# Optimization experiments

Measured on AMD Instinct MI355X. Metric: run time of the kernel, lower is better.

## Reference

```python
import jax, jax.numpy as jnp
import numpy as np


def setup_inputs() -> dict:
    key = jax.random.key(0)
    ks = jax.random.split(key, 7)
    n, d_in, d_h = 1024, 1024, 512
    scale = 1.0 / np.sqrt(d_in)
    return {
        "vectors": jax.random.normal(ks[0], (n, d_in), dtype=jnp.float32),
        "W_h": jax.random.normal(ks[1], (d_h, d_in), dtype=jnp.float32) * scale,
        "b_h": jax.random.normal(ks[2], (d_h,), dtype=jnp.float32) * 0.01,
        "W_m": jax.random.normal(ks[3], (d_h, d_in), dtype=jnp.float32) * scale,
        "b_m": jax.random.normal(ks[4], (d_h,), dtype=jnp.float32) * 0.01,
        "w2": jax.random.normal(ks[5], (d_h,), dtype=jnp.float32) * (1.0 / np.sqrt(d_h)),
        "b2": jax.random.normal(ks[6], (1,), dtype=jnp.float32) * 0.01,
    }


def reference(vectors, W_h, b_h, W_m, b_m, w2, b2):
    # Two linear projections: [n, d_h]
    h = vectors @ W_h.T + b_h  # head representations
    m = vectors @ W_m.T + b_m  # modifier representations
    # Pairwise broadcast add: pair[i, j, :] = h[i] + m[j]  -> [n, n, d_h]
    pair = jnp.tanh(h[:, None, :] + m[None, :, :])
    # Linear to scalar + squeeze -> [n, n]
    scores = jnp.einsum("ijh,h->ij", pair, w2) + b2[0]
    return scores
```

## Files before the change

### kernel.cpp

```cpp
#include <hip/hip_runtime.h>
#include <hip/hip_bf16.h>

#define D_IN  1024
#define D_H   512
#define L2E2  2.885390081777927f
#define ECLAMP 15.0f

typedef _Float16 half8 __attribute__((ext_vector_type(8)));
typedef _Float16 half4v __attribute__((ext_vector_type(4)));
typedef float f32x4 __attribute__((ext_vector_type(4)));

__global__ __launch_bounds__(256) void cvt_kernel(
    const float* __restrict__ V,
    const float* __restrict__ Wh, const float* __restrict__ Wm,
    _Float16* __restrict__ Vh, _Float16* __restrict__ Wf)
{
  const int idx = blockIdx.x * 256 + threadIdx.x;
  {
    float4 x = ((const float4*)V)[idx];
    half4v o = { (_Float16)x.x, (_Float16)x.y, (_Float16)x.z, (_Float16)x.w };
    ((half4v*)Vh)[idx] = o;
  }
  {
    const float4* p = (idx < 131072) ? ((const float4*)Wh + idx)
                                     : ((const float4*)Wm + (idx - 131072));
    float4 x = *p;
    half4v o = { (_Float16)x.x, (_Float16)x.y, (_Float16)x.z, (_Float16)x.w };
    ((half4v*)Wf)[idx] = o;
  }
}

__global__ __launch_bounds__(256, 4) void proj_mfma_kernel(
    const _Float16* __restrict__ Vh, const _Float16* __restrict__ Wf,
    const float* __restrict__ bh, const float* __restrict__ bm,
    float* __restrict__ C)
{
  __shared__ float red[4][32][34];

  const int tid  = threadIdx.x;
  const int lane = tid & 63;
  const int wid  = tid >> 6;
  const int bid  = blockIdx.x;
  const int swz  = (bid & 7) * 128 + (bid >> 3);
  const int i0   = (swz & 31) * 32;
  const int j0   = (swz >> 5) * 32;
  const int r16  = lane & 15;
  const int kg   = lane >> 4;
  const int kb   = wid * 256;

  const _Float16* A0 = Vh + (size_t)(i0 + r16) * 1024 + kb + kg*8;
  const _Float16* A1 = A0 + 16 * 1024;
  const _Float16* B0 = Wf + (size_t)(j0 + r16) * 1024 + kb + kg*8;
  const _Float16* B1 = B0 + 16 * 1024;

  f32x4 acc00 = {0.f,0.f,0.f,0.f}, acc01 = acc00, acc10 = acc00, acc11 = acc00;
  #pragma unroll 4
  for (int k0 = 0; k0 < 256; k0 += 32) {
    half8 a0 = *(const half8*)(A0 + k0);
    half8 a1 = *(const half8*)(A1 + k0);
    half8 b0 = *(const half8*)(B0 + k0);
    half8 b1 = *(const half8*)(B1 + k0);
    acc00 = __builtin_amdgcn_mfma_f32_16x16x32_f16(a0, b0, acc00, 0, 0, 0);
    acc01 = __builtin_amdgcn_mfma_f32_16x16x32_f16(a0, b1, acc01, 0, 0, 0);
    acc10 = __builtin_amdgcn_mfma_f32_16x16x32_f16(a1, b0, acc10, 0, 0, 0);
    acc11 = __builtin_amdgcn_mfma_f32_16x16x32_f16(a1, b1, acc11, 0, 0, 0);
  }

  #pragma unroll
  for (int fi = 0; fi < 2; ++fi) {
    #pragma unroll
    for (int fj = 0; fj < 2; ++fj) {
      const f32x4 acc = (fi == 0) ? (fj == 0 ? acc00 : acc01)
                                  : (fj == 0 ? acc10 : acc11);
      #pragma unroll
      for (int rr = 0; rr < 4; ++rr)
        red[wid][16*fi + 4*kg + rr][16*fj + r16] = acc[rr];
    }
  }
  __syncthreads();

  const int row = tid >> 3;
  const int c4  = (tid & 7) * 4;
  const float* biasp = (j0 < D_H) ? (bh + j0) : (bm + (j0 - D_H));
  float4 bias = *(const float4*)(biasp + c4);
  float4 o;
  #pragma unroll
  for (int q = 0; q < 4; ++q) {
    float s = red[0][row][c4+q] + red[1][row][c4+q]
            + red[2][row][c4+q] + red[3][row][c4+q];
    float x = (s + (&bias.x)[q]) * L2E2;
    x = fminf(fmaxf(x, -ECLAMP), ECLAMP);
    (&o.x)[q] = __builtin_amdgcn_exp2f(x);
  }
  *(float4*)(C + (size_t)(i0 + row) * 1024 + j0 + c4) = o;
}

__global__ __launch_bounds__(256) void proj_kernel(
    const float* __restrict__ V,
    const float* __restrict__ Wh, const float* __restrict__ bh,
    const float* __restrict__ Wm, const float* __restrict__ bm,
    float* __restrict__ C)
{
  __shared__ float As[16][68];
  __shared__ float Bs[16][68];

  const int tid = threadIdx.x;
  const int i0  = (blockIdx.x & 15) * 64, j0 = (blockIdx.x >> 4) * 64;
  const int ti  = tid >> 4, tj = tid & 15;
  const int sr  = tid >> 2;
  const int sk  = (tid & 3) << 2;

  const float* Wbase = (j0 < D_H) ? (Wh + (size_t)j0 * D_IN)
                                  : (Wm + (size_t)(j0 - D_H) * D_IN);
  const float* biasp = (j0 < D_H) ? (bh + j0) : (bm + (j0 - D_H));

  const float* arow = V     + (size_t)(i0 + sr) * D_IN + sk;
  const float* brow = Wbase + (size_t)sr        * D_IN + sk;

  float acc[4][4] = {};
  for (int k0 = 0; k0 < D_IN; k0 += 16) {
    float4 av = *(const float4*)(arow + k0);
    float4 bv = *(const float4*)(brow + k0);
    As[sk+0][sr] = av.x; As[sk+1][sr] = av.y; As[sk+2][sr] = av.z; As[sk+3][sr] = av.w;
    Bs[sk+0][sr] = bv.x; Bs[sk+1][sr] = bv.y; Bs[sk+2][sr] = bv.z; Bs[sk+3][sr] = bv.w;
    __syncthreads();
    #pragma unroll
    for (int kk = 0; kk < 16; ++kk) {
      float4 a = *(const float4*)&As[kk][4*ti];
      float4 b = *(const float4*)&Bs[kk][4*tj];
      #pragma unroll
      for (int x = 0; x < 4; ++x)
        #pragma unroll
        for (int y = 0; y < 4; ++y)
          acc[x][y] = fmaf((&a.x)[x], (&b.x)[y], acc[x][y]);
    }
    __syncthreads();
  }

  const int jl = 4 * tj;
  #pragma unroll
  for (int aa = 0; aa < 4; ++aa) {
    const int i = i0 + 4*ti + aa;
    float4 o;
    #pragma unroll
    for (int bb = 0; bb < 4; ++bb) {
      float x = (acc[aa][bb] + biasp[jl+bb]) * L2E2;
      x = fminf(fmaxf(x, -ECLAMP), ECLAMP);
      (&o.x)[bb] = __builtin_amdgcn_exp2f(x);
    }
    *(float4*)(C + (size_t)i * 1024 + j0 + jl) = o;
  }
}

__global__ __launch_bounds__(256, 2) void score_kernel(
    const float* __restrict__ C,
    const float* __restrict__ w2,
    const float* __restrict__ b2,
    float* __restrict__ out)
{
  __shared__ float hs[2][64][34];
  __shared__ float ms[2][32][34];
  __shared__ float wred[4];

  const int tid = threadIdx.x;
  const int bi  = blockIdx.x & 15;
  const int bj  = blockIdx.x >> 4;
  const int i0  = bi * 64, j0 = bj * 32;
  const int ti  = tid >> 4, tj = tid & 15;

  const int sr  = tid >> 3;
  const int sk  = (tid & 7) << 2;

  float sw = 0.f;
  for (int t = tid; t < D_H; t += 256) sw += w2[t];
  #pragma unroll
  for (int off = 32; off > 0; off >>= 1) sw += __shfl_down(sw, off, 64);
  if ((tid & 63) == 0) wred[tid >> 6] = sw;

  const float* hrow0 = C + (size_t)(i0 + sr)      * 1024 + sk;
  const float* hrow1 = C + (size_t)(i0 + sr + 32) * 1024 + sk;
  const float* mrow  = C + (size_t)(j0 + sr) * 1024 + D_H + sk;

  float4 hv0 = *(const float4*)(hrow0);
  float4 hv1 = *(const float4*)(hrow1);
  float4 mv  = *(const float4*)(mrow);

  float acc[4][2] = {};
  int p = 0;

  for (int k0 = 0; k0 < D_H; k0 += 32) {
    *(float2*)&hs[p][sr][sk]          = make_float2(hv0.x, hv0.y);
    *(float2*)&hs[p][sr][sk + 2]      = make_float2(hv0.z, hv0.w);
    *(float2*)&hs[p][sr + 32][sk]     = make_float2(hv1.x, hv1.y);
    *(float2*)&hs[p][sr + 32][sk + 2] = make_float2(hv1.z, hv1.w);
    *(float2*)&ms[p][sr][sk]          = make_float2(mv.x, mv.y);
    *(float2*)&ms[p][sr][sk + 2]      = make_float2(mv.z, mv.w);
    __syncthreads();

    if (k0 + 32 < D_H) {
      hv0 = *(const float4*)(hrow0 + k0 + 32);
      hv1 = *(const float4*)(hrow1 + k0 + 32);
      mv  = *(const float4*)(mrow  + k0 + 32);
    }

    #pragma unroll
    for (int g = 0; g < 8; ++g) {
      const int kk = 4 * g;
      const float wA = w2[k0 + kk + 0];
      const float wB = w2[k0 + kk + 1];
      const float wC = w2[k0 + kk + 2];
      const float wD = w2[k0 + kk + 3];
      float2 em_[2][2], eh_[4][2];
      #pragma unroll
      for (int c = 0; c < 2; ++c) {
        em_[c][0] = *(const float2*)&ms[p][tj + 16*c][kk];
        em_[c][1] = *(const float2*)&ms[p][tj + 16*c][kk + 2];
      }
      #pragma unroll
      for (int a = 0; a < 4; ++a) {
        eh_[a][0] = *(const float2*)&hs[p][ti + 16*a][kk];
        eh_[a][1] = *(const float2*)&hs[p][ti + 16*a][kk + 2];
      }
      #pragma unroll
      for (int a = 0; a < 4; ++a)
        #pragma unroll
        for (int c = 0; c < 2; ++c) {
          float uA = fmaf(eh_[a][0].x, em_[c][0].x, 1.f);
          float uB = fmaf(eh_[a][0].y, em_[c][0].y, 1.f);
          float uC = fmaf(eh_[a][1].x, em_[c][1].x, 1.f);
          float uD = fmaf(eh_[a][1].y, em_[c][1].y, 1.f);
          float dAB = uA * uB, dCD = uC * uD;
          float nAB = fmaf(wB, uA, wA * uB);
          float nCD = fmaf(wD, uC, wC * uD);
          float den = dAB * dCD;
          float num = fmaf(nCD, dAB, nAB * dCD);
          acc[a][c] = fmaf(num, __builtin_amdgcn_rcpf(den), acc[a][c]);
        }
    }
    p ^= 1;
  }

  const float base = b2[0] + wred[0] + wred[1] + wred[2] + wred[3];
  #pragma unroll
  for (int a = 0; a < 4; ++a) {
    const int i = i0 + ti + 16*a;
    #pragma unroll
    for (int c = 0; c < 2; ++c) {
      const int j = j0 + tj + 16*c;
      out[(size_t)i * 1024 + j] = fmaf(-2.f, acc[a][c], base);
    }
  }
}

extern "C" void kernel_launch(void* const* d_in, const int* in_sizes, int n_in,
                              void* d_out, int out_size, void* d_ws, size_t ws_size,
                              hipStream_t stream) {
  const float* V  = (const float*)d_in[0];
  const float* Wh = (const float*)d_in[1];
  const float* bh = (const float*)d_in[2];
  const float* Wm = (const float*)d_in[3];
  const float* bm = (const float*)d_in[4];
  const float* w2 = (const float*)d_in[5];
  const float* b2 = (const float*)d_in[6];
  float* outp = (float*)d_out;

  char* ws = (char*)d_ws;
  float* C = (float*)ws;

  if (ws_size >= (size_t)(8u << 20)) {
    _Float16* Vh = (_Float16*)(ws + (4u << 20));
    _Float16* Wf = (_Float16*)(ws + (6u << 20));
    cvt_kernel<<<dim3(1024), dim3(256), 0, stream>>>(V, Wh, Wm, Vh, Wf);
    proj_mfma_kernel<<<dim3(1024), dim3(256), 0, stream>>>(Vh, Wf, bh, bm, C);
  } else {
    proj_kernel<<<dim3(256), dim3(256), 0, stream>>>(V, Wh, bh, Wm, bm, C);
  }
  score_kernel<<<dim3(512), dim3(256), 0, stream>>>(C, w2, b2, outp);
}
```

Before: 80.94 us.

## Fuse fp16 conversion into projection and split score reduction over hidden dim

Removes the separate conversion kernel: the MFMA projection now loads fp32 inputs and converts to fp16 in registers. The score kernel is split four ways along the hidden dimension with 64x64 tiles and 1024 blocks, each writing fp16 partial sums that a new combine kernel adds into the output. This aims to raise parallelism and per-thread reuse in the dominant score stage. The cost is an extra launch, partial-sum memory traffic, and precision loss from storing partials in fp16.

Measured after the change: 85.35 us. +5.5%, slower.

```diff
diff --git a/kernel.cpp b/kernel.cpp
--- a/kernel.cpp
+++ b/kernel.cpp
@@ -10,28 +10,18 @@
 typedef _Float16 half4v __attribute__((ext_vector_type(4)));
 typedef float f32x4 __attribute__((ext_vector_type(4)));
 
-__global__ __launch_bounds__(256) void cvt_kernel(
+static __device__ __forceinline__ half8 cvt8(float4 lo, float4 hi) {
+  half8 r;
+  r[0] = (_Float16)lo.x; r[1] = (_Float16)lo.y;
+  r[2] = (_Float16)lo.z; r[3] = (_Float16)lo.w;
+  r[4] = (_Float16)hi.x; r[5] = (_Float16)hi.y;
+  r[6] = (_Float16)hi.z; r[7] = (_Float16)hi.w;
+  return r;
+}
+
+__global__ __launch_bounds__(256, 2) void proj_fused_kernel(
     const float* __restrict__ V,
     const float* __restrict__ Wh, const float* __restrict__ Wm,
-    _Float16* __restrict__ Vh, _Float16* __restrict__ Wf)
-{
-  const int idx = blockIdx.x * 256 + threadIdx.x;
-  {
-    float4 x = ((const float4*)V)[idx];
-    half4v o = { (_Float16)x.x, (_Float16)x.y, (_Float16)x.z, (_Float16)x.w };
-    ((half4v*)Vh)[idx] = o;
-  }
-  {
-    const float4* p = (idx < 131072) ? ((const float4*)Wh + idx)
-                                     : ((const float4*)Wm + (idx - 131072));
-    float4 x = *p;
-    half4v o = { (_Float16)x.x, (_Float16)x.y, (_Float16)x.z, (_Float16)x.w };
-    ((half4v*)Wf)[idx] = o;
-  }
-}
-
-__global__ __launch_bounds__(256, 4) void proj_mfma_kernel(
-    const _Float16* __restrict__ Vh, const _Float16* __restrict__ Wf,
     const float* __restrict__ bh, const float* __restrict__ bm,
     float* __restrict__ C)
 {
@@ -48,18 +38,21 @@
   const int kg   = lane >> 4;
   const int kb   = wid * 256;
 
-  const _Float16* A0 = Vh + (size_t)(i0 + r16) * 1024 + kb + kg*8;
-  const _Float16* A1 = A0 + 16 * 1024;
-  const _Float16* B0 = Wf + (size_t)(j0 + r16) * 1024 + kb + kg*8;
-  const _Float16* B1 = B0 + 16 * 1024;
+  const float* Wbase = (j0 < D_H) ? (Wh + (size_t)j0 * D_IN)
+                                  : (Wm + (size_t)(j0 - D_H) * D_IN);
+
+  const float* A0 = V     + (size_t)(i0 + r16) * 1024 + kb + kg*8;
+  const float* A1 = A0 + 16 * 1024;
+  const float* B0 = Wbase + (size_t)r16        * 1024 + kb + kg*8;
+  const float* B1 = B0 + 16 * 1024;
 
   f32x4 acc00 = {0.f,0.f,0.f,0.f}, acc01 = acc00, acc10 = acc00, acc11 = acc00;
   #pragma unroll 4
   for (int k0 = 0; k0 < 256; k0 += 32) {
-    half8 a0 = *(const half8*)(A0 + k0);
-    half8 a1 = *(const half8*)(A1 + k0);
-    half8 b0 = *(const half8*)(B0 + k0);
-    half8 b1 = *(const half8*)(B1 + k0);
+    half8 a0 = cvt8(*(const float4*)(A0 + k0), *(const float4*)(A0 + k0 + 4));
+    half8 a1 = cvt8(*(const float4*)(A1 + k0), *(const float4*)(A1 + k0 + 4));
+    half8 b0 = cvt8(*(const float4*)(B0 + k0), *(const float4*)(B0 + k0 + 4));
+    half8 b1 = cvt8(*(const float4*)(B1 + k0), *(const float4*)(B1 + k0 + 4));
     acc00 = __builtin_amdgcn_mfma_f32_16x16x32_f16(a0, b0, acc00, 0, 0, 0);
     acc01 = __builtin_amdgcn_mfma_f32_16x16x32_f16(a0, b1, acc01, 0, 0, 0);
     acc10 = __builtin_amdgcn_mfma_f32_16x16x32_f16(a1, b0, acc10, 0, 0, 0);
@@ -95,140 +88,88 @@
   *(float4*)(C + (size_t)(i0 + row) * 1024 + j0 + c4) = o;
 }
 
-__global__ __launch_bounds__(256) void proj_kernel(
-    const float* __restrict__ V,
-    const float* __restrict__ Wh, const float* __restrict__ bh,
-    const float* __restrict__ Wm, const float* __restrict__ bm,
-    float* __restrict__ C)
-{
-  __shared__ float As[16][68];
-  __shared__ float Bs[16][68];
-
-  const int tid = threadIdx.x;
-  const int i0  = (blockIdx.x & 15) * 64, j0 = (blockIdx.x >> 4) * 64;
-  const int ti  = tid >> 4, tj = tid & 15;
-  const int sr  = tid >> 2;
-  const int sk  = (tid & 3) << 2;
-
-  const float* Wbase = (j0 < D_H) ? (Wh + (size_t)j0 * D_IN)
-                                  : (Wm + (size_t)(j0 - D_H) * D_IN);
-  const float* biasp = (j0 < D_H) ? (bh + j0) : (bm + (j0 - D_H));
-
-  const float* arow = V     + (size_t)(i0 + sr) * D_IN + sk;
-  const float* brow = Wbase + (size_t)sr        * D_IN + sk;
-
-  float acc[4][4] = {};
-  for (int k0 = 0; k0 < D_IN; k0 += 16) {
-    float4 av = *(const float4*)(arow + k0);
-    float4 bv = *(const float4*)(brow + k0);
-    As[sk+0][sr] = av.x; As[sk+1][sr] = av.y; As[sk+2][sr] = av.z; As[sk+3][sr] = av.w;
-    Bs[sk+0][sr] = bv.x; Bs[sk+1][sr] = bv.y; Bs[sk+2][sr] = bv.z; Bs[sk+3][sr] = bv.w;
-    __syncthreads();
-    #pragma unroll
-    for (int kk = 0; kk < 16; ++kk) {
-      float4 a = *(const float4*)&As[kk][4*ti];
-      float4 b = *(const float4*)&Bs[kk][4*tj];
-      #pragma unroll
-      for (int x = 0; x < 4; ++x)
-        #pragma unroll
-        for (int y = 0; y < 4; ++y)
-          acc[x][y] = fmaf((&a.x)[x], (&b.x)[y], acc[x][y]);
-    }
-    __syncthreads();
-  }
-
-  const int jl = 4 * tj;
-  #pragma unroll
-  for (int aa = 0; aa < 4; ++aa) {
-    const int i = i0 + 4*ti + aa;
-    float4 o;
-    #pragma unroll
-    for (int bb = 0; bb < 4; ++bb) {
-      float x = (acc[aa][bb] + biasp[jl+bb]) * L2E2;
-      x = fminf(fmaxf(x, -ECLAMP), ECLAMP);
-      (&o.x)[bb] = __builtin_amdgcn_exp2f(x);
-    }
-    *(float4*)(C + (size_t)i * 1024 + j0 + jl) = o;
-  }
-}
-
-__global__ __launch_bounds__(256, 2) void score_kernel(
+__global__ __launch_bounds__(256, 2) void score_q_kernel(
     const float* __restrict__ C,
     const float* __restrict__ w2,
     const float* __restrict__ b2,
-    float* __restrict__ out)
+    _Float16* __restrict__ P0, _Float16* __restrict__ P1,
+    _Float16* __restrict__ P2, _Float16* __restrict__ P3)
 {
-  __shared__ float hs[2][64][34];
-  __shared__ float ms[2][32][34];
+  __shared__ float hs[2][64][36];
+  __shared__ float ms[2][64][36];
   __shared__ float wred[4];
 
-  const int tid = threadIdx.x;
-  const int bi  = blockIdx.x & 15;
-  const int bj  = blockIdx.x >> 4;
-  const int i0  = bi * 64, j0 = bj * 32;
-  const int ti  = tid >> 4, tj = tid & 15;
-
-  const int sr  = tid >> 3;
-  const int sk  = (tid & 7) << 2;
-
-  float sw = 0.f;
-  for (int t = tid; t < D_H; t += 256) sw += w2[t];
-  #pragma unroll
-  for (int off = 32; off > 0; off >>= 1) sw += __shfl_down(sw, off, 64);
-  if ((tid & 63) == 0) wred[tid >> 6] = sw;
-
-  const float* hrow0 = C + (size_t)(i0 + sr)      * 1024 + sk;
-  const float* hrow1 = C + (size_t)(i0 + sr + 32) * 1024 + sk;
-  const float* mrow  = C + (size_t)(j0 + sr) * 1024 + D_H + sk;
+  const int tid  = threadIdx.x;
+  const int b    = blockIdx.x;
+  const int v    = (b & 7) * 128 + (b >> 3);
+  const int tile = v >> 2;
+  const int kh   = v & 3;
+  const int i0   = (tile & 15) * 64;
+  const int j0   = (tile >> 4) * 64;
+  const int kb   = kh * 128;
+  const int ti   = tid >> 4, tj = tid & 15;
+
+  const int sr   = tid >> 3;
+  const int sk   = (tid & 7) << 2;
+
+  if (kh == 0) {
+    float sw = 0.f;
+    for (int t = tid; t < D_H; t += 256) sw += w2[t];
+    #pragma unroll
+    for (int off = 32; off > 0; off >>= 1) sw += __shfl_down(sw, off, 64);
+    if ((tid & 63) == 0) wred[tid >> 6] = sw;
+  }
+
+  const float* hrow0 = C + (size_t)(i0 + sr)      * 1024 + kb + sk;
+  const float* hrow1 = C + (size_t)(i0 + sr + 32) * 1024 + kb + sk;
+  const float* mrow0 = C + (size_t)(j0 + sr)      * 1024 + D_H + kb + sk;
+  const float* mrow1 = C + (size_t)(j0 + sr + 32) * 1024 + D_H + kb + sk;
 
   float4 hv0 = *(const float4*)(hrow0);
   float4 hv1 = *(const float4*)(hrow1);
-  float4 mv  = *(const float4*)(mrow);
-
-  float acc[4][2] = {};
+  float4 mv0 = *(const float4*)(mrow0);
+  float4 mv1 = *(const float4*)(mrow1);
+
+  float acc[4][4] = {};
   int p = 0;
 
-  for (int k0 = 0; k0 < D_H; k0 += 32) {
-    *(float2*)&hs[p][sr][sk]          = make_float2(hv0.x, hv0.y);
-    *(float2*)&hs[p][sr][sk + 2]      = make_float2(hv0.z, hv0.w);
-    *(float2*)&hs[p][sr + 32][sk]     = make_float2(hv1.x, hv1.y);
-    *(float2*)&hs[p][sr + 32][sk + 2] = make_float2(hv1.z, hv1.w);
-    *(float2*)&ms[p][sr][sk]          = make_float2(mv.x, mv.y);
-    *(float2*)&ms[p][sr][sk + 2]      = make_float2(mv.z, mv.w);
+  for (int k0 = 0; k0 < 128; k0 += 32) {
+    *(float4*)&hs[p][sr][sk]      = hv0;
+    *(float4*)&hs[p][sr + 32][sk] = hv1;
+    *(float4*)&ms[p][sr][sk]      = mv0;
+    *(float4*)&ms[p][sr + 32][sk] = mv1;
     __syncthreads();
 
-    if (k0 + 32 < D_H) {
+    if (k0 + 32 < 128) {
       hv0 = *(const float4*)(hrow0 + k0 + 32);
       hv1 = *(const float4*)(hrow1 + k0 + 32);
-      mv  = *(const float4*)(mrow  + k0 + 32);
+      mv0 = *(const float4*)(mrow0 + k0 + 32);
+      mv1 = *(const float4*)(mrow1 + k0 + 32);
     }
 
     #pragma unroll
     for (int g = 0; g < 8; ++g) {
       const int kk = 4 * g;
-      const float wA = w2[k0 + kk + 0];
-      const float wB = w2[k0 + kk + 1];
-      const float wC = w2[k0 + kk + 2];
-      const float wD = w2[k0 + kk + 3];
-      float2 em_[2][2], eh_[4][2];
-      #pragma unroll
-      for (int c = 0; c < 2; ++c) {
-        em_[c][0] = *(const float2*)&ms[p][tj + 16*c][kk];
-        em_[c][1] = *(const float2*)&ms[p][tj + 16*c][kk + 2];
-      }
+      float4 eh[4], em[4];
+      #pragma unroll
+      for (int a = 0; a < 4; ++a)
+        eh[a] = *(const float4*)&hs[p][ti + 16*a][kk];
+      #pragma unroll
+      for (int c = 0; c < 4; ++c)
+        em[c] = *(const float4*)&ms[p][tj + 16*c][kk];
+
+      const float wA = w2[kb + k0 + kk + 0];
+      const float wB = w2[kb + k0 + kk + 1];
+      const float wC = w2[kb + k0 + kk + 2];
+      const float wD = w2[kb + k0 + kk + 3];
       #pragma unroll
       for (int a = 0; a < 4; ++a) {
-        eh_[a][0] = *(const float2*)&hs[p][ti + 16*a][kk];
-        eh_[a][1] = *(const float2*)&hs[p][ti + 16*a][kk + 2];
-      }
-      #pragma unroll
-      for (int a = 0; a < 4; ++a)
         #pragma unroll
-        for (int c = 0; c < 2; ++c) {
-          float uA = fmaf(eh_[a][0].x, em_[c][0].x, 1.f);
-          float uB = fmaf(eh_[a][0].y, em_[c][0].y, 1.f);
-          float uC = fmaf(eh_[a][1].x, em_[c][1].x, 1.f);
-          float uD = fmaf(eh_[a][1].y, em_[c][1].y, 1.f);
+        for (int c = 0; c < 4; ++c) {
+          float uA = fmaf(eh[a].x, em[c].x, 1.f);
+          float uB = fmaf(eh[a].y, em[c].y, 1.f);
+          float uC = fmaf(eh[a].z, em[c].z, 1.f);
+          float uD = fmaf(eh[a].w, em[c].w, 1.f);
           float dAB = uA * uB, dCD = uC * uD;
           float nAB = fmaf(wB, uA, wA * uB);
           float nCD = fmaf(wD, uC, wC * uD);
@@ -236,6 +177,122 @@
           float num = fmaf(nCD, dAB, nAB * dCD);
           acc[a][c] = fmaf(num, __builtin_amdgcn_rcpf(den), acc[a][c]);
         }
+      }
+    }
+    p ^= 1;
+  }
+
+  float base = 0.f;
+  if (kh == 0) base = b2[0] + wred[0] + wred[1] + wred[2] + wred[3];
+  _Float16* Pz = (kh == 0) ? P0 : (kh == 1) ? P1 : (kh == 2) ? P2 : P3;
+  #pragma unroll
+  for (int a = 0; a < 4; ++a) {
+    const int i = i0 + ti + 16*a;
+    #pragma unroll
+    for (int c = 0; c < 4; ++c) {
+      const int j = j0 + tj + 16*c;
+      Pz[(size_t)i * 1024 + j] = (_Float16)fmaf(-2.f, acc[a][c], base);
+    }
+  }
+}
+
+__global__ __launch_bounds__(256) void combine_kernel(
+    const _Float16* __restrict__ P0, const _Float16* __restrict__ P1,
+    const _Float16* __restrict__ P2, const _Float16* __restrict__ P3,
+    float* __restrict__ out)
+{
+  const int idx = blockIdx.x * 256 + threadIdx.x;
+  half4v a = ((const half4v*)P0)[idx];
+  half4v b = ((const half4v*)P1)[idx];
+  half4v c = ((const half4v*)P2)[idx];
+  half4v d = ((const half4v*)P3)[idx];
+  float4 o;
+  #pragma unroll
+  for (int q = 0; q < 4; ++q)
+    (&o.x)[q] = (float)a[q] + (float)b[q] + ((float)c[q] + (float)d[q]);
+  ((float4*)out)[idx] = o;
+}
+
+__global__ __launch_bounds__(256, 2) void score_kernel_r9(
+    const float* __restrict__ C,
+    const float* __restrict__ w2,
+    const float* __restrict__ b2,
+    float* __restrict__ out)
+{
+  __shared__ float hs[2][64][36];
+  __shared__ float ms[2][32][36];
+  __shared__ float wred[4];
+
+  const int tid = threadIdx.x;
+  const int bi  = blockIdx.x & 15;
+  const int bj  = blockIdx.x >> 4;
+  const int i0  = bi * 64, j0 = bj * 32;
+  const int ti  = tid >> 4, tj = tid & 15;
+
+  const int sr  = tid >> 3;
+  const int sk  = (tid & 7) << 2;
+
+  float sw = 0.f;
+  for (int t = tid; t < D_H; t += 256) sw += w2[t];
+  #pragma unroll
+  for (int off = 32; off > 0; off >>= 1) sw += __shfl_down(sw, off, 64);
+  if ((tid & 63) == 0) wred[tid >> 6] = sw;
+
+  const float* hrow0 = C + (size_t)(i0 + sr)      * 1024 + sk;
+  const float* hrow1 = C + (size_t)(i0 + sr + 32) * 1024 + sk;
+  const float* mrow  = C + (size_t)(j0 + sr) * 1024 + D_H + sk;
+
+  float4 hv0 = *(const float4*)(hrow0);
+  float4 hv1 = *(const float4*)(hrow1);
+  float4 mv  = *(const float4*)(mrow);
+
+  float acc[4][2] = {};
+  int p = 0;
+
+  for (int k0 = 0; k0 < D_H; k0 += 32) {
+    *(float4*)&hs[p][sr][sk]      = hv0;
+    *(float4*)&hs[p][sr + 32][sk] = hv1;
+    *(float4*)&ms[p][sr][sk]      = mv;
+    __syncthreads();
+
+    if (k0 + 32 < D_H) {
+      hv0 = *(const float4*)(hrow0 + k0 + 32);
+      hv1 = *(const float4*)(hrow1 + k0 + 32);
+      mv  = *(const float4*)(mrow  + k0 + 32);
+    }
+
+    #pragma unroll
+    for (int g = 0; g < 8; ++g) {
+      const int kk = 4 * g;
+      float4 eh[4];
+      float4 em[2];
+      #pragma unroll
+      for (int a = 0; a < 4; ++a)
+        eh[a] = *(const float4*)&hs[p][ti + 16*a][kk];
+      #pragma unroll
+      for (int c = 0; c < 2; ++c)
+        em[c] = *(const float4*)&ms[p][tj + 16*c][kk];
+
+      const float wA = w2[k0 + kk + 0];
+      const float wB = w2[k0 + kk + 1];
+      const float wC = w2[k0 + kk + 2];
+      const float wD = w2[k0 + kk + 3];
+      #pragma unroll
+      for (int a = 0; a < 4; ++a) {
+        #pragma unroll
+        for (int c = 0; c < 2; ++c) {
+          float uA = fmaf(eh[a].x, em[c].x, 1.f);
+          float uB = fmaf(eh[a].y, em[c].y, 1.f);
+          float uC = fmaf(eh[a].z, em[c].z, 1.f);
+          float uD = fmaf(eh[a].w, em[c].w, 1.f);
+          float dAB = uA * uB, dCD = uC * uD;
+          float nAB = fmaf(wB, uA, wA * uB);
+          float nCD = fmaf(wD, uC, wC * uD);
+          float den = dAB * dCD;
+          float num = fmaf(nCD, dAB, nAB * dCD);
+          acc[a][c] = fmaf(num, __builtin_amdgcn_rcpf(den), acc[a][c]);
+        }
+      }
     }
     p ^= 1;
   }
@@ -267,13 +324,16 @@
   char* ws = (char*)d_ws;
   float* C = (float*)ws;
 
-  if (ws_size >= (size_t)(8u << 20)) {
-    _Float16* Vh = (_Float16*)(ws + (4u << 20));
-    _Float16* Wf = (_Float16*)(ws + (6u << 20));
-    cvt_kernel<<<dim3(1024), dim3(256), 0, stream>>>(V, Wh, Wm, Vh, Wf);
-    proj_mfma_kernel<<<dim3(1024), dim3(256), 0, stream>>>(Vh, Wf, bh, bm, C);
+  proj_fused_kernel<<<dim3(1024), dim3(256), 0, stream>>>(V, Wh, Wm, bh, bm, C);
+
+  if (ws_size >= (size_t)(12u << 20)) {
+    _Float16* P0 = (_Float16*)(ws + (4u << 20));
+    _Float16* P1 = (_Float16*)(ws + (6u << 20));
+    _Float16* P2 = (_Float16*)(ws + (8u << 20));
+    _Float16* P3 = (_Float16*)(ws + (10u << 20));
+    score_q_kernel<<<dim3(1024), dim3(256), 0, stream>>>(C, w2, b2, P0, P1, P2, P3);
+    combine_kernel<<<dim3(1024), dim3(256), 0, stream>>>(P0, P1, P2, P3, outp);
   } else {
-    proj_kernel<<<dim3(256), dim3(256), 0, stream>>>(V, Wh, bh, Wm, bm, C);
-  }
-  score_kernel<<<dim3(512), dim3(256), 0, stream>>>(C, w2, b2, outp);
-}
+    score_kernel_r9<<<dim3(512), dim3(256), 0, stream>>>(C, w2, b2, outp);
+  }
+}
```

## Split score reduction over hidden dim into four partial kernels plus combine

Applied to the files above, without the earlier changes.

Adds a split-K score kernel. Each of 1024 blocks computes a 64x64 output tile over a quarter of the hidden dimension, reading operands straight from global memory without LDS, and writes fp16 partial sums. A combine kernel then adds the four partials into the fp32 output. This raises parallelism and drops LDS staging and barriers, at the cost of an extra launch, extra partial traffic, and fp16 rounding of partials, which risks accuracy. The fallback score kernel also switches to float4 LDS accesses with padding changed to 36.

After: 105.7 us. 1.31x slower.

```diff
diff --git a/kernel.cpp b/kernel.cpp
--- a/kernel.cpp
+++ b/kernel.cpp
@@ -152,14 +152,111 @@
   }
 }
 
-__global__ __launch_bounds__(256, 2) void score_kernel(
+__global__ __launch_bounds__(256, 2) void score_gd_kernel(
+    const float* __restrict__ C,
+    const float* __restrict__ w2,
+    const float* __restrict__ b2,
+    _Float16* __restrict__ P0, _Float16* __restrict__ P1,
+    _Float16* __restrict__ P2, _Float16* __restrict__ P3)
+{
+  __shared__ float wred[4];
+
+  const int tid  = threadIdx.x;
+  const int b    = blockIdx.x;
+  const int v    = (b & 7) * 128 + (b >> 3);
+  const int tile = v >> 2;
+  const int kh   = v & 3;
+  const int i0   = (tile & 15) * 64;
+  const int j0   = (tile >> 4) * 64;
+  const int kb   = kh * 128;
+  const int ti   = tid >> 4, tj = tid & 15;
+
+  if (kh == 0) {
+    float sw = 0.f;
+    for (int t = tid; t < D_H; t += 256) sw += w2[t];
+    #pragma unroll
+    for (int off = 32; off > 0; off >>= 1) sw += __shfl_down(sw, off, 64);
+    if ((tid & 63) == 0) wred[tid >> 6] = sw;
+  }
+  __syncthreads();
+
+  const float* ehb = C + (size_t)(i0 + ti) * 1024 + kb;
+  const float* emb = C + (size_t)(j0 + tj) * 1024 + D_H + kb;
+
+  float acc[4][4] = {};
+
+  #pragma unroll 4
+  for (int g = 0; g < 32; ++g) {
+    const int kk = 4 * g;
+    float4 eh[4], em[4];
+    #pragma unroll
+    for (int a = 0; a < 4; ++a)
+      eh[a] = *(const float4*)(ehb + (size_t)a * 16384 + kk);
+    #pragma unroll
+    for (int c = 0; c < 4; ++c)
+      em[c] = *(const float4*)(emb + (size_t)c * 16384 + kk);
+
+    const float wA = w2[kb + kk + 0];
+    const float wB = w2[kb + kk + 1];
+    const float wC = w2[kb + kk + 2];
+    const float wD = w2[kb + kk + 3];
+    #pragma unroll
+    for (int a = 0; a < 4; ++a) {
+      #pragma unroll
+      for (int c = 0; c < 4; ++c) {
+        float uA = fmaf(eh[a].x, em[c].x, 1.f);
+        float uB = fmaf(eh[a].y, em[c].y, 1.f);
+        float uC = fmaf(eh[a].z, em[c].z, 1.f);
+        float uD = fmaf(eh[a].w, em[c].w, 1.f);
+        float dAB = uA * uB, dCD = uC * uD;
+        float nAB = fmaf(wB, uA, wA * uB);
+        float nCD = fmaf(wD, uC, wC * uD);
+        float den = dAB * dCD;
+        float num = fmaf(nCD, dAB, nAB * dCD);
+        acc[a][c] = fmaf(num, __builtin_amdgcn_rcpf(den), acc[a][c]);
+      }
+    }
+  }
+
+  float base = 0.f;
+  if (kh == 0) base = b2[0] + wred[0] + wred[1] + wred[2] + wred[3];
+  _Float16* Pz = (kh == 0) ? P0 : (kh == 1) ? P1 : (kh == 2) ? P2 : P3;
+  #pragma unroll
+  for (int a = 0; a < 4; ++a) {
+    const int i = i0 + ti + 16*a;
+    #pragma unroll
+    for (int c = 0; c < 4; ++c) {
+      const int j = j0 + tj + 16*c;
+      Pz[(size_t)i * 1024 + j] = (_Float16)fmaf(-2.f, acc[a][c], base);
+    }
+  }
+}
+
+__global__ __launch_bounds__(256) void combine_kernel(
+    const _Float16* __restrict__ P0, const _Float16* __restrict__ P1,
+    const _Float16* __restrict__ P2, const _Float16* __restrict__ P3,
+    float* __restrict__ out)
+{
+  const int idx = blockIdx.x * 256 + threadIdx.x;
+  half4v a = ((const half4v*)P0)[idx];
+  half4v b = ((const half4v*)P1)[idx];
+  half4v c = ((const half4v*)P2)[idx];
+  half4v d = ((const half4v*)P3)[idx];
+  float4 o;
+  #pragma unroll
+  for (int q = 0; q < 4; ++q)
+    (&o.x)[q] = (float)a[q] + (float)b[q] + ((float)c[q] + (float)d[q]);
+  ((float4*)out)[idx] = o;
+}
+
+__global__ __launch_bounds__(256, 2) void score_kernel_r9(
     const float* __restrict__ C,
     const float* __restrict__ w2,
     const float* __restrict__ b2,
     float* __restrict__ out)
 {
-  __shared__ float hs[2][64][34];
-  __shared__ float ms[2][32][34];
+  __shared__ float hs[2][64][36];
+  __shared__ float ms[2][32][36];
   __shared__ float wred[4];
 
   const int tid = threadIdx.x;
@@ -189,12 +286,9 @@
   int p = 0;
 
   for (int k0 = 0; k0 < D_H; k0 += 32) {
-    *(float2*)&hs[p][sr][sk]          = make_float2(hv0.x, hv0.y);
-    *(float2*)&hs[p][sr][sk + 2]      = make_float2(hv0.z, hv0.w);
-    *(float2*)&hs[p][sr + 32][sk]     = make_float2(hv1.x, hv1.y);
-    *(float2*)&hs[p][sr + 32][sk + 2] = make_float2(hv1.z, hv1.w);
-    *(float2*)&ms[p][sr][sk]          = make_float2(mv.x, mv.y);
-    *(float2*)&ms[p][sr][sk + 2]      = make_float2(mv.z, mv.w);
+    *(float4*)&hs[p][sr][sk]      = hv0;
+    *(float4*)&hs[p][sr + 32][sk] = hv1;
+    *(float4*)&ms[p][sr][sk]      = mv;
     __syncthreads();
 
     if (k0 + 32 < D_H) {
@@ -206,29 +300,27 @@
     #pragma unroll
     for (int g = 0; g < 8; ++g) {
       const int kk = 4 * g;
+      float4 eh[4];
+      float4 em[2];
+      #pragma unroll
+      for (int a = 0; a < 4; ++a)
+        eh[a] = *(const float4*)&hs[p][ti + 16*a][kk];
+      #pragma unroll
+      for (int c = 0; c < 2; ++c)
+        em[c] = *(const float4*)&ms[p][tj + 16*c][kk];
+
       const float wA = w2[k0 + kk + 0];
       const float wB = w2[k0 + kk + 1];
       const float wC = w2[k0 + kk + 2];
       const float wD = w2[k0 + kk + 3];
-      float2 em_[2][2], eh_[4][2];
-      #pragma unroll
-      for (int c = 0; c < 2; ++c) {
-        em_[c][0] = *(const float2*)&ms[p][tj + 16*c][kk];
-        em_[c][1] = *(const float2*)&ms[p][tj + 16*c][kk + 2];
-      }
       #pragma unroll
       for (int a = 0; a < 4; ++a) {
-        eh_[a][0] = *(const float2*)&hs[p][ti + 16*a][kk];
-        eh_[a][1] = *(const float2*)&hs[p][ti + 16*a][kk + 2];
-      }
-      #pragma unroll
-      for (int a = 0; a < 4; ++a)
         #pragma unroll
         for (int c = 0; c < 2; ++c) {
-          float uA = fmaf(eh_[a][0].x, em_[c][0].x, 1.f);
-          float uB = fmaf(eh_[a][0].y, em_[c][0].y, 1.f);
-          float uC = fmaf(eh_[a][1].x, em_[c][1].x, 1.f);
-          float uD = fmaf(eh_[a][1].y, em_[c][1].y, 1.f);
+          float uA = fmaf(eh[a].x, em[c].x, 1.f);
+          float uB = fmaf(eh[a].y, em[c].y, 1.f);
+          float uC = fmaf(eh[a].z, em[c].z, 1.f);
+          float uD = fmaf(eh[a].w, em[c].w, 1.f);
           float dAB = uA * uB, dCD = uC * uD;
           float nAB = fmaf(wB, uA, wA * uB);
           float nCD = fmaf(wD, uC, wC * uD);
@@ -236,6 +328,7 @@
           float num = fmaf(nCD, dAB, nAB * dCD);
           acc[a][c] = fmaf(num, __builtin_amdgcn_rcpf(den), acc[a][c]);
         }
+      }
     }
     p ^= 1;
   }
@@ -267,13 +360,25 @@
   char* ws = (char*)d_ws;
   float* C = (float*)ws;
 
-  if (ws_size >= (size_t)(8u << 20)) {
+  if (ws_size >= (size_t)(16u << 20)) {
+    _Float16* Vh = (_Float16*)(ws + (4u << 20));
+    _Float16* Wf = (_Float16*)(ws + (6u << 20));
+    _Float16* P0 = (_Float16*)(ws + (8u << 20));
+    _Float16* P1 = (_Float16*)(ws + (10u << 20));
+    _Float16* P2 = (_Float16*)(ws + (12u << 20));
+    _Float16* P3 = (_Float16*)(ws + (14u << 20));
+    cvt_kernel<<<dim3(1024), dim3(256), 0, stream>>>(V, Wh, Wm, Vh, Wf);
+    proj_mfma_kernel<<<dim3(1024), dim3(256), 0, stream>>>(Vh, Wf, bh, bm, C);
+    score_gd_kernel<<<dim3(1024), dim3(256), 0, stream>>>(C, w2, b2, P0, P1, P2, P3);
+    combine_kernel<<<dim3(1024), dim3(256), 0, stream>>>(P0, P1, P2, P3, outp);
+  } else if (ws_size >= (size_t)(8u << 20)) {
     _Float16* Vh = (_Float16*)(ws + (4u << 20));
     _Float16* Wf = (_Float16*)(ws + (6u << 20));
     cvt_kernel<<<dim3(1024), dim3(256), 0, stream>>>(V, Wh, Wm, Vh, Wf);
     proj_mfma_kernel<<<dim3(1024), dim3(256), 0, stream>>>(Vh, Wf, bh, bm, C);
+    score_kernel_r9<<<dim3(512), dim3(256), 0, stream>>>(C, w2, b2, outp);
   } else {
     proj_kernel<<<dim3(256), dim3(256), 0, stream>>>(V, Wh, bh, Wm, bm, C);
-  }
-  score_kernel<<<dim3(512), dim3(256), 0, stream>>>(C, w2, b2, outp);
-}
+    score_kernel_r9<<<dim3(512), dim3(256), 0, stream>>>(C, w2, b2, outp);
+  }
+}
```
